# Optimization experiments

Hardware: AMD Instinct MI355X
Metric: run time of the kernel (lower is better)

Reference implementation:

```python
import jax, jax.numpy as jnp
import numpy as np
from jax import lax

B = 8      # batch size
R = 64     # voxel grid resolution
DN = ('NDHWC', 'DHWIO', 'NDHWC')  # conv dimension numbers


def setup_inputs() -> dict:
    key = jax.random.key(0)
    ks = jax.random.split(key, 8)
    N = 200000
    # coords: (batch, x, y, z). Sparse active voxels.
    b = jax.random.randint(ks[0], (N, 1), 0, B, dtype=jnp.int32)
    xyz = jax.random.randint(ks[1], (N, 3), 0, R, dtype=jnp.int32)
    coords = jnp.concatenate([b, xyz], axis=1)
    feats = jax.random.normal(ks[2], (N, 1), dtype=jnp.float32)
    W1 = jax.random.normal(ks[3], (3, 3, 3, 1, 32), dtype=jnp.float32) * 0.2
    W2 = jax.random.normal(ks[4], (2, 2, 2, 32, 64), dtype=jnp.float32) * 0.1
    W3 = jax.random.normal(ks[5], (2, 2, 2, 64, 128), dtype=jnp.float32) * 0.07
    fc_w = jax.random.normal(ks[6], (128, 256), dtype=jnp.float32) * 0.09
    fc_b = jnp.zeros((256,), dtype=jnp.float32)
    return {"coords": coords, "feats": feats, "W1": W1, "W2": W2,
            "W3": W3, "fc_w": fc_w, "fc_b": fc_b}


def _pool_mask(m):
    # active-site mask after a stride-2 kernel-2 sparse conv: any active input
    # voxel in the 2x2x2 block activates the output site.
    return lax.reduce_window(m, 0.0, lax.max, (1, 2, 2, 2, 1), (1, 2, 2, 2, 1), 'VALID')


def reference(coords, feats, W1, W2, W3, fc_w, fc_b):
    b, x, y, z = coords[:, 0], coords[:, 1], coords[:, 2], coords[:, 3]
    # Densify the sparse tensor (duplicate coords summed for determinism)
    grid = jnp.zeros((B, R, R, R, 1), feats.dtype).at[b, x, y, z].add(feats)
    mask = jnp.zeros((B, R, R, R, 1), feats.dtype).at[b, x, y, z].set(1.0)

    # Conv3d(1,32,k=3,s=1): submanifold -> output coords == input coords (mask)
    h = lax.conv_general_dilated(grid, W1, (1, 1, 1), 'SAME', dimension_numbers=DN)
    h = jax.nn.relu(h) * mask

    # Conv3d(32,64,k=2,s=2): downsample; active iff any active input in block
    h = lax.conv_general_dilated(h, W2, (2, 2, 2), 'VALID', dimension_numbers=DN)
    mask2 = _pool_mask(mask)
    h = jax.nn.relu(h) * mask2

    # Conv3d(64,128,k=2,s=2)
    h = lax.conv_general_dilated(h, W3, (2, 2, 2), 'VALID', dimension_numbers=DN)
    mask3 = _pool_mask(mask2)
    h = jax.nn.relu(h) * mask3

    # GlobalAvgPool over ACTIVE voxels only, per batch
    s = jnp.sum(h, axis=(1, 2, 3))                       # [B,128]
    cnt = jnp.sum(mask3, axis=(1, 2, 3))                 # [B,1]
    pooled = s / jnp.maximum(cnt, 1.0)

    return pooled @ fc_w + fc_b                          # [B,256]
```

## Files before the change

### kernel.cpp

```cpp
#include <hip/hip_runtime.h>
#include <hip/hip_bf16.h>
#include <hip/hip_fp16.h>

typedef __attribute__((ext_vector_type(2))) _Float16 f16x2;
typedef __attribute__((ext_vector_type(8))) _Float16 f16x8;
typedef __attribute__((ext_vector_type(4))) float    f32x4;

#define GRID_ELEMS (8*64*64*64)
#define ZERO_U4    540800

__global__ __launch_bounds__(256) void zero_k(uint4* __restrict__ p)
{
  const unsigned i = blockIdx.x * 256 + threadIdx.x;
  if (i < ZERO_U4) p[i] = (uint4){0u, 0u, 0u, 0u};
}

__global__ __launch_bounds__(256) void scatter_setup_k(
    const int* __restrict__ coords, const float* __restrict__ feats,
    const float* __restrict__ W1, const float* __restrict__ W2, const float* __restrict__ W3,
    __half2* __restrict__ gpk,
    uint4* __restrict__ W1f, uint4* __restrict__ W2f,
    uint4* __restrict__ W3fA, uint4* __restrict__ W3fB, int N)
{
  const int bi = blockIdx.x;
  if (bi < 44) {
    const int i = bi * 256 + threadIdx.x;
    if (i < 2048) {
      const int wid = i >> 9, ks = (i >> 6) & 7, lane = i & 63;
      const int l15 = lane & 15, l4 = lane >> 4, o = wid * 16 + l15;
      f16x8 v;
      #pragma unroll
      for (int j = 0; j < 8; ++j)
        v[j] = (_Float16)W2[ks * 2048 + (l4 * 8 + j) * 64 + o];
      W2f[i] = __builtin_bit_cast(uint4, v);
    } else if (i < 10240) {
      const int e = i - 2048, ab = e >> 12, r = e & 4095;
      const int wid = r >> 10, ks = (r >> 6) & 15, lane = r & 63;
      const int l15 = lane & 15, l4 = lane >> 4, o = wid * 32 + l15 + ab * 16;
      f16x8 v;
      #pragma unroll
      for (int j = 0; j < 8; ++j)
        v[j] = (_Float16)W3[(ks >> 1) * 8192 + ((ks & 1) * 32 + l4 * 8 + j) * 128 + o];
      (ab ? W3fB : W3fA)[r] = __builtin_bit_cast(uint4, v);
    } else if (i < 10368) {
      const int t = i - 10240;
      const int mt = t >> 6, l = t & 63;
      f16x8 v;
      #pragma unroll
      for (int j = 0; j < 8; ++j) {
        const int k = (l >> 4) * 8 + j;
        v[j] = (k < 27) ? (_Float16)W1[k * 32 + mt * 16 + (l & 15)] : (_Float16)0;
      }
      W1f[t] = __builtin_bit_cast(uint4, v);
    }
    return;
  }
  const int i = (bi - 44) * 256 + threadIdx.x;
  if (i >= N) return;
  const int4 c = reinterpret_cast<const int4*>(coords)[i];
  const int idx = ((c.x * 64 + c.y) * 64 + c.z) * 64 + c.w;
  const __half2 v = __halves2half2(__float2half_rn(feats[i]), __float2half_rn(1.0f));
  unsafeAtomicAdd(&gpk[idx], v);
}

__global__ __launch_bounds__(256, 4) void mega_k(
    const unsigned* __restrict__ gpk,
    const uint4* __restrict__ W1f, const uint4* __restrict__ W2f,
    const uint4* __restrict__ W3fA, const uint4* __restrict__ W3fB,
    float* __restrict__ spart, float* __restrict__ cntB)
{
  __shared__ __align__(16) char smem[35920];
  _Float16* const h1f  = (_Float16*)(smem + 11264);
  _Float16* const tile = (_Float16*)(smem + 27648);
  float*    const m1v  = (float*)(smem + 31248);
  float*    const m2s  = (float*)(smem + 35344);
  float*    const m3s  = (float*)(smem + 35856);

  const int tid = threadIdx.x;
  const int bid = blockIdx.x;
  const int b   = bid >> 8;
  const int X2  = (bid >> 5) & 7, Y2 = (bid >> 2) & 7, Zp = bid & 3;
  const int gb  = b << 18;
  const int lane = tid & 63, wid = tid >> 6;
  const int l15 = lane & 15, l4 = lane >> 4;

  {
    const int gx0 = X2 * 8 - 1, gy0 = Y2 * 8 - 1, gz0 = Zp * 16 - 1;
    for (int e = tid; e < 1800; e += 256) {
      const int x = e / 180, r = e - x * 180, y = r / 18, z = r - y * 18;
      const int gx = gx0 + x, gy = gy0 + y, gz = gz0 + z;
      const bool ok = ((unsigned)gx < 64u) & ((unsigned)gy < 64u) & ((unsigned)gz < 64u);
      const unsigned g = ok ? gpk[gb + (gx << 12) + (gy << 6) + gz] : 0u;
      tile[e] = __builtin_bit_cast(_Float16, (unsigned short)(g & 0xffffu));
      const int ix = x - 1, iy = y - 1, iz = z - 1;
      if (((unsigned)ix < 8u) & ((unsigned)iy < 8u) & ((unsigned)iz < 16u))
        m1v[(ix << 7) + (iy << 4) + iz] = (g >> 16) ? 1.f : 0.f;
    }
  }

  const uint4 w1a = W1f[lane];
  const uint4 w1b = W1f[64 + lane];
  uint4 w2r[8];
  #pragma unroll
  for (int ks = 0; ks < 8; ++ks) w2r[ks] = W2f[(wid * 8 + ks) * 64 + lane];

  int t_off[8];
  #pragma unroll
  for (int j = 0; j < 8; ++j) {
    const int k = l4 * 8 + j;
    int off = 0;
    if (k < 27) {
      const int tx = k / 9, rr = k - 9 * tx, ty = rr / 3, tz = rr - 3 * ty;
      off = (tx * 180 + ty * 18 + tz) * 2;
    }
    t_off[j] = off;
  }

  __syncthreads();

  if (tid < 128) {
    const int base = ((tid >> 5) << 8) + (((tid >> 3) & 3) << 5) + ((tid & 7) << 1);
    float m = m1v[base];
    m = fmaxf(m, m1v[base + 1]);   m = fmaxf(m, m1v[base + 16]);
    m = fmaxf(m, m1v[base + 17]);  m = fmaxf(m, m1v[base + 128]);
    m = fmaxf(m, m1v[base + 129]); m = fmaxf(m, m1v[base + 144]);
    m = fmaxf(m, m1v[base + 145]);
    m2s[tid] = m;
  }

  const char* tilec = (const char*)tile;
  uint4 wa[4], wb2[4];

  #pragma unroll
  for (int o = 0; o < 2; ++o) {
    f32x4 acc[4];
    #pragma unroll
    for (int nt = 0; nt < 4; ++nt) acc[nt] = (f32x4){0.f, 0.f, 0.f, 0.f};

    #pragma unroll
    for (int cc = 0; cc < 2; ++cc) {
      #pragma unroll
      for (int gi = 0; gi < 4; ++gi) {
        const int idx = (wid * 4 + gi) * 16 + l15;
        const int x1 = 2 * (idx >> 6) + cc, y1 = (idx >> 3) & 7, zo = idx & 7;
        const int z1 = o * 8 + zo;
        const int base2 = (x1 * 180 + y1 * 18 + z1) * 2;
        f16x8 bf;
        #pragma unroll
        for (int j = 0; j < 8; ++j)
          bf[j] = *reinterpret_cast<const _Float16*>(tilec + base2 + t_off[j]);
        f32x4 aA = (f32x4){0.f, 0.f, 0.f, 0.f};
        f32x4 aB = (f32x4){0.f, 0.f, 0.f, 0.f};
        aA = __builtin_amdgcn_mfma_f32_16x16x32_f16(__builtin_bit_cast(f16x8, w1a), bf, aA, 0, 0, 0);
        aB = __builtin_amdgcn_mfma_f32_16x16x32_f16(__builtin_bit_cast(f16x8, w1b), bf, aB, 0, 0, 0);

        const unsigned umask = (m1v[(x1 << 7) + (y1 << 4) + z1] != 0.f) ? 0xffffffffu : 0u;
        const int p_l = ((y1 & 1) << 1) | (zo & 1);
        const int v2  = ((x1 >> 1) << 4) | ((y1 >> 1) << 2) | (zo >> 1);
        const int fbase = (((v2 >> 4) * 4 + p_l) * 64 + (v2 & 15)) * 8 + (l4 & 1) * 4;
        const int qsel = l4 >> 1;
        uint2 wA, wB;
        {
          const auto c0 = __builtin_amdgcn_cvt_pkrtz(fmaxf(aA[0], 0.f), fmaxf(aA[1], 0.f));
          const auto c1 = __builtin_amdgcn_cvt_pkrtz(fmaxf(aA[2], 0.f), fmaxf(aA[3], 0.f));
          wA.x = __builtin_bit_cast(unsigned, c0) & umask;
          wA.y = __builtin_bit_cast(unsigned, c1) & umask;
        }
        {
          const auto c0 = __builtin_amdgcn_cvt_pkrtz(fmaxf(aB[0], 0.f), fmaxf(aB[1], 0.f));
          const auto c1 = __builtin_amdgcn_cvt_pkrtz(fmaxf(aB[2], 0.f), fmaxf(aB[3], 0.f));
          wB.x = __builtin_bit_cast(unsigned, c0) & umask;
          wB.y = __builtin_bit_cast(unsigned, c1) & umask;
        }
        *reinterpret_cast<uint2*>(&h1f[fbase + qsel * 128])       = wA;
        *reinterpret_cast<uint2*>(&h1f[fbase + (2 + qsel) * 128]) = wB;
      }
      __syncthreads();

      if (o == 0 && cc == 0 && tid < 16) {
        const int base = ((tid >> 3) << 6) + (((tid >> 2) & 1) << 4) + ((tid & 3) << 1);
        float m = m2s[base];
        m = fmaxf(m, m2s[base + 1]);  m = fmaxf(m, m2s[base + 8]);
        m = fmaxf(m, m2s[base + 9]);  m = fmaxf(m, m2s[base + 32]);
        m = fmaxf(m, m2s[base + 33]); m = fmaxf(m, m2s[base + 40]);
        m = fmaxf(m, m2s[base + 41]);
        m3s[tid] = m;
      }

      #pragma unroll
      for (int ks = 0; ks < 4; ++ks) {
        const f16x8 af = __builtin_bit_cast(f16x8, w2r[cc * 4 + ks]);
        #pragma unroll
        for (int nt = 0; nt < 4; ++nt) {
          const f16x8 bb = *reinterpret_cast<const f16x8*>(&h1f[((nt * 4 + ks) * 64 + lane) * 8]);
          acc[nt] = __builtin_amdgcn_mfma_f32_16x16x32_f16(af, bb, acc[nt], 0, 0, 0);
        }
      }

      if (o == 1 && cc == 1) {
        #pragma unroll
        for (int j = 0; j < 4; ++j) {
          wa[j]  = W3fA[(wid * 16 + j) * 64 + lane];
          wb2[j] = W3fB[(wid * 16 + j) * 64 + lane];
        }
      }
      __syncthreads();
    }

    _Float16* const h2o = (_Float16*)(smem + o * 11264);
    const int o0 = wid * 16 + l4 * 4;
    #pragma unroll
    for (int nt = 0; nt < 4; ++nt) {
      const int v2l = nt * 16 + l15;
      const float m2v = m2s[((v2l >> 4) << 5) + (((v2l >> 2) & 3) << 3) + o * 4 + (v2l & 3)];
      const unsigned um = (m2v != 0.f) ? 0xffffffffu : 0u;
      const auto p0 = __builtin_amdgcn_cvt_pkrtz(fmaxf(acc[nt][0], 0.f), fmaxf(acc[nt][1], 0.f));
      const auto p1 = __builtin_amdgcn_cvt_pkrtz(fmaxf(acc[nt][2], 0.f), fmaxf(acc[nt][3], 0.f));
      uint2 u;
      u.x = __builtin_bit_cast(unsigned, p0) & um;
      u.y = __builtin_bit_cast(unsigned, p1) & um;
      *reinterpret_cast<uint2*>(&h2o[v2l * 88 + o0]) = u;
    }
  }
  __syncthreads();

  f32x4 c3a = (f32x4){0.f,0.f,0.f,0.f};
  f32x4 c3b = (f32x4){0.f,0.f,0.f,0.f};
  const int v3 = l15;
  const int x3 = v3 >> 3, y3 = (v3 >> 2) & 1, z3 = v3 & 3;
  const int obyte = (z3 >> 1) * 11264;

  #pragma unroll
  for (int kc = 0; kc < 4; ++kc) {
    uint4 na[4], nb[4];
    if (kc < 3) {
      #pragma unroll
      for (int j = 0; j < 4; ++j) {
        na[j] = W3fA[(wid * 16 + (kc + 1) * 4 + j) * 64 + lane];
        nb[j] = W3fB[(wid * 16 + (kc + 1) * 4 + j) * 64 + lane];
      }
    }
    #pragma unroll
    for (int j = 0; j < 4; ++j) {
      const int ks = kc * 4 + j;
      const int p = ks >> 1;
      const int x2 = 2 * x3 + (p >> 2), y2 = 2 * y3 + ((p >> 1) & 1);
      const int z2l = 2 * (z3 & 1) + (p & 1);
      const int v2l = (x2 << 4) | (y2 << 2) | z2l;
      const int c0 = (ks & 1) * 32 + l4 * 8;
      const f16x8 bf = *reinterpret_cast<const f16x8*>(smem + obyte + (v2l * 88 + c0) * 2);
      c3a = __builtin_amdgcn_mfma_f32_16x16x32_f16(__builtin_bit_cast(f16x8, wa[j]),  bf, c3a, 0, 0, 0);
      c3b = __builtin_amdgcn_mfma_f32_16x16x32_f16(__builtin_bit_cast(f16x8, wb2[j]), bf, c3b, 0, 0, 0);
    }
    if (kc < 3) {
      #pragma unroll
      for (int j = 0; j < 4; ++j) { wa[j] = na[j]; wb2[j] = nb[j]; }
    }
  }

  const float m3v = m3s[v3];
  float part[2][4];
  #pragma unroll
  for (int j = 0; j < 4; ++j) {
    part[0][j] = fmaxf(c3a[j], 0.f) * m3v;
    part[1][j] = fmaxf(c3b[j], 0.f) * m3v;
  }
  #pragma unroll
  for (int d = 1; d < 16; d <<= 1) {
    #pragma unroll
    for (int mt = 0; mt < 2; ++mt)
      #pragma unroll
      for (int j = 0; j < 4; ++j)
        part[mt][j] += __shfl_xor(part[mt][j], d, 64);
  }
  if (l15 == 0) {
    const int sb = (b * 64 + (bid & 63)) * 128 + wid * 32;
    #pragma unroll
    for (int mt = 0; mt < 2; ++mt)
      #pragma unroll
      for (int j = 0; j < 4; ++j)
        atomicAdd(&spart[sb + mt * 16 + l4 * 4 + j], part[mt][j]);
  }
  if (tid == 0) {
    float t = 0.f;
    #pragma unroll
    for (int i = 0; i < 16; ++i) t += m3s[i];
    atomicAdd(&cntB[b * 64 + (bid & 63)], t);
  }
}

__global__ __launch_bounds__(256) void reduce_fc_k(
    const float* __restrict__ spart, const float* __restrict__ cntB,
    const float* __restrict__ fc_w, const float* __restrict__ fc_b,
    float* __restrict__ out)
{
  __shared__ float s_l[128];
  __shared__ float c_l;
  const int b = blockIdx.x, tid = threadIdx.x;
  if (tid < 128) {
    float a = 0.f;
    #pragma unroll 8
    for (int g = 0; g < 64; ++g) a += spart[(b * 64 + g) * 128 + tid];
    s_l[tid] = a;
  } else if (tid < 192) {
    float a = cntB[b * 64 + (tid - 128)];
    #pragma unroll
    for (int d = 1; d < 64; d <<= 1) a += __shfl_xor(a, d, 64);
    if (tid == 128) c_l = a;
  }
  __syncthreads();
  const float inv = 1.f / fmaxf(c_l, 1.f);
  float o = fc_b[tid];
  #pragma unroll 8
  for (int c = 0; c < 128; ++c) o = fmaf(s_l[c] * inv, fc_w[c * 256 + tid], o);
  out[b * 256 + tid] = o;
}

extern "C" void kernel_launch(void* const* d_in, const int* in_sizes, int n_in,
                              void* d_out, int out_size, void* d_ws, size_t ws_size,
                              hipStream_t stream)
{
  const int*   coords = (const int*)  d_in[0];
  const float* feats  = (const float*)d_in[1];
  const float* W1     = (const float*)d_in[2];
  const float* W2     = (const float*)d_in[3];
  const float* W3     = (const float*)d_in[4];
  const float* fc_w   = (const float*)d_in[5];
  const float* fc_b   = (const float*)d_in[6];
  float* out = (float*)d_out;
  const int N = in_sizes[0] / 4;

  unsigned* gpk   = (unsigned*)d_ws;
  float*    spart = (float*)(gpk + GRID_ELEMS);
  float*    cntB  = spart + 8 * 64 * 128;
  uint4*    W1f   = (uint4*)(cntB + 512);
  uint4*    W2f   = W1f + 128;
  uint4*    W3fA  = W2f + 2048;
  uint4*    W3fB  = W3fA + 4096;

  zero_k<<<(ZERO_U4 + 255) / 256, 256, 0, stream>>>((uint4*)gpk);
  scatter_setup_k<<<44 + (N + 255) / 256, 256, 0, stream>>>(
      coords, feats, W1, W2, W3, (__half2*)gpk, W1f, W2f, W3fA, W3fB, N);
  mega_k<<<2048, 256, 0, stream>>>(gpk, W1f, W2f, W3fA, W3fB, spart, cntB);
  reduce_fc_k<<<8, 256, 0, stream>>>(spart, cntB, fc_w, fc_b, out);
}
```

Baseline: 69.07 us.

## Compact active voxels into per-phase lists and skip inactive conv1 MFMA work

During tile load, the kernel builds per-(z-half, x-parity) byte lists of occupied level-1 voxels in LDS using shared atomics. Conv1 then iterates only over groups of 16 active voxels instead of all 256 sites per phase, after zero-filling the h1 buffer so inactive sites read as zero. This is meant to cut MFMA and gather work in the sparse first conv stage. In exchange it adds LDS atomics, a zero-fill pass, an extra barrier, and load imbalance across waves.

```diff
diff --git a/kernel.cpp b/kernel.cpp
--- a/kernel.cpp
+++ b/kernel.cpp
@@ -69,12 +69,14 @@
     const uint4* __restrict__ W3fA, const uint4* __restrict__ W3fB,
     float* __restrict__ spart, float* __restrict__ cntB)
 {
-  __shared__ __align__(16) char smem[35920];
+  __shared__ __align__(16) char smem[36960];
   _Float16* const h1f  = (_Float16*)(smem + 11264);
   _Float16* const tile = (_Float16*)(smem + 27648);
   float*    const m1v  = (float*)(smem + 31248);
   float*    const m2s  = (float*)(smem + 35344);
   float*    const m3s  = (float*)(smem + 35856);
+  unsigned char* const lists = (unsigned char*)(smem + 35920);
+  int*      const lcnt = (int*)(smem + 36944);
 
   const int tid = threadIdx.x;
   const int bid = blockIdx.x;
@@ -83,6 +85,9 @@
   const int gb  = b << 18;
   const int lane = tid & 63, wid = tid >> 6;
   const int l15 = lane & 15, l4 = lane >> 4;
+
+  if (tid < 4) lcnt[tid] = 0;
+  __syncthreads();
 
   {
     const int gx0 = X2 * 8 - 1, gy0 = Y2 * 8 - 1, gz0 = Zp * 16 - 1;
@@ -93,8 +98,16 @@
       const unsigned g = ok ? gpk[gb + (gx << 12) + (gy << 6) + gz] : 0u;
       tile[e] = __builtin_bit_cast(_Float16, (unsigned short)(g & 0xffffu));
       const int ix = x - 1, iy = y - 1, iz = z - 1;
-      if (((unsigned)ix < 8u) & ((unsigned)iy < 8u) & ((unsigned)iz < 16u))
-        m1v[(ix << 7) + (iy << 4) + iz] = (g >> 16) ? 1.f : 0.f;
+      if (((unsigned)ix < 8u) & ((unsigned)iy < 8u) & ((unsigned)iz < 16u)) {
+        const bool occ = (g >> 16) != 0u;
+        m1v[(ix << 7) + (iy << 4) + iz] = occ ? 1.f : 0.f;
+        if (occ) {
+          const int li = ((iz >> 3) << 1) | (ix & 1);
+          const int slot = atomicAdd(&lcnt[li], 1);
+          lists[li * 256 + slot] =
+              (unsigned char)(((ix >> 1) << 6) | (iy << 3) | (iz & 7));
+        }
+      }
     }
   }
 
@@ -139,9 +152,18 @@
 
     #pragma unroll
     for (int cc = 0; cc < 2; ++cc) {
-      #pragma unroll
-      for (int gi = 0; gi < 4; ++gi) {
-        const int idx = (wid * 4 + gi) * 16 + l15;
+      {
+        uint4* zp = reinterpret_cast<uint4*>((char*)h1f + tid * 64);
+        const uint4 z4 = (uint4){0u, 0u, 0u, 0u};
+        zp[0] = z4; zp[1] = z4; zp[2] = z4; zp[3] = z4;
+      }
+      __syncthreads();
+
+      const int lc = lcnt[o * 2 + cc];
+      for (int g = wid; g * 16 < lc; g += 4) {
+        const int slot = g * 16 + l15;
+        const bool valid = slot < lc;
+        const int idx = valid ? (int)lists[(o * 2 + cc) * 256 + slot] : 0;
         const int x1 = 2 * (idx >> 6) + cc, y1 = (idx >> 3) & 7, zo = idx & 7;
         const int z1 = o * 8 + zo;
         const int base2 = (x1 * 180 + y1 * 18 + z1) * 2;
@@ -154,26 +176,27 @@
         aA = __builtin_amdgcn_mfma_f32_16x16x32_f16(__builtin_bit_cast(f16x8, w1a), bf, aA, 0, 0, 0);
         aB = __builtin_amdgcn_mfma_f32_16x16x32_f16(__builtin_bit_cast(f16x8, w1b), bf, aB, 0, 0, 0);
 
-        const unsigned umask = (m1v[(x1 << 7) + (y1 << 4) + z1] != 0.f) ? 0xffffffffu : 0u;
-        const int p_l = ((y1 & 1) << 1) | (zo & 1);
-        const int v2  = ((x1 >> 1) << 4) | ((y1 >> 1) << 2) | (zo >> 1);
-        const int fbase = (((v2 >> 4) * 4 + p_l) * 64 + (v2 & 15)) * 8 + (l4 & 1) * 4;
-        const int qsel = l4 >> 1;
-        uint2 wA, wB;
-        {
-          const auto c0 = __builtin_amdgcn_cvt_pkrtz(fmaxf(aA[0], 0.f), fmaxf(aA[1], 0.f));
-          const auto c1 = __builtin_amdgcn_cvt_pkrtz(fmaxf(aA[2], 0.f), fmaxf(aA[3], 0.f));
-          wA.x = __builtin_bit_cast(unsigned, c0) & umask;
-          wA.y = __builtin_bit_cast(unsigned, c1) & umask;
+        if (valid) {
+          const int p_l = ((y1 & 1) << 1) | (zo & 1);
+          const int v2  = ((x1 >> 1) << 4) | ((y1 >> 1) << 2) | (zo >> 1);
+          const int fbase = (((v2 >> 4) * 4 + p_l) * 64 + (v2 & 15)) * 8 + (l4 & 1) * 4;
+          const int qsel = l4 >> 1;
+          uint2 wA, wB;
+          {
+            const auto c0 = __builtin_amdgcn_cvt_pkrtz(fmaxf(aA[0], 0.f), fmaxf(aA[1], 0.f));
+            const auto c1 = __builtin_amdgcn_cvt_pkrtz(fmaxf(aA[2], 0.f), fmaxf(aA[3], 0.f));
+            wA.x = __builtin_bit_cast(unsigned, c0);
+            wA.y = __builtin_bit_cast(unsigned, c1);
+          }
+          {
+            const auto c0 = __builtin_amdgcn_cvt_pkrtz(fmaxf(aB[0], 0.f), fmaxf(aB[1], 0.f));
+            const auto c1 = __builtin_amdgcn_cvt_pkrtz(fmaxf(aB[2], 0.f), fmaxf(aB[3], 0.f));
+            wB.x = __builtin_bit_cast(unsigned, c0);
+            wB.y = __builtin_bit_cast(unsigned, c1);
+          }
+          *reinterpret_cast<uint2*>(&h1f[fbase + qsel * 128])       = wA;
+          *reinterpret_cast<uint2*>(&h1f[fbase + (2 + qsel) * 128]) = wB;
         }
-        {
-          const auto c0 = __builtin_amdgcn_cvt_pkrtz(fmaxf(aB[0], 0.f), fmaxf(aB[1], 0.f));
-          const auto c1 = __builtin_amdgcn_cvt_pkrtz(fmaxf(aB[2], 0.f), fmaxf(aB[3], 0.f));
-          wB.x = __builtin_bit_cast(unsigned, c0) & umask;
-          wB.y = __builtin_bit_cast(unsigned, c1) & umask;
-        }
-        *reinterpret_cast<uint2*>(&h1f[fbase + qsel * 128])       = wA;
-        *reinterpret_cast<uint2*>(&h1f[fbase + (2 + qsel) * 128]) = wB;
       }
       __syncthreads();
 
```

Measured after the change: 65.59 us, median of 2. 1.05x faster.
